# Optimization experiments

Measured on AMD Instinct MI355X. Metric: run time of the kernel, lower is better.

The kernel has to match this reference:

```python
import jax, jax.numpy as jnp
import numpy as np

N_NODES = 50000
N_EDGES = 800000
IN_CH = 128
HID_CH = 128


def glorot(key, shape):
    fan_in, fan_out = shape[0], shape[1]
    lim = np.sqrt(6.0 / (fan_in + fan_out)).astype(np.float32)
    return jax.random.uniform(key, shape, jnp.float32, -lim, lim)


def setup_inputs() -> dict:
    key = jax.random.key(0)
    k1, k2, k3, k4 = jax.random.split(key, 4)
    x = jax.random.normal(k1, (N_NODES, IN_CH), jnp.float32)
    edge_index = jax.random.randint(k2, (2, N_EDGES), 0, N_NODES, jnp.int64)
    W1 = glorot(k3, (IN_CH, HID_CH))
    b1 = jnp.zeros((HID_CH,), jnp.float32)
    W2 = glorot(k4, (HID_CH, HID_CH))
    b2 = jnp.zeros((HID_CH,), jnp.float32)
    return {"x": x, "edge_index": edge_index, "W1": W1, "b1": b1, "W2": W2, "b2": b2}


def _gcn_conv(x, W, b, src, dst, n_nodes):
    # PyG GCNConv: h = D^{-1/2} (A + I) D^{-1/2} (x W) + b
    h = x @ W  # [N, H] transform first (as in PyG)
    loops = jnp.arange(n_nodes, dtype=src.dtype)
    s = jnp.concatenate([src, loops])  # add self-loops
    d = jnp.concatenate([dst, loops])
    deg = jnp.zeros((n_nodes,), h.dtype).at[d].add(1.0)
    dinv = jnp.where(deg > 0, jax.lax.rsqrt(deg), 0.0)
    coef = dinv[s] * dinv[d]  # [E+N]
    msg = h[s] * coef[:, None]  # gather + scale
    out = jax.ops.segment_sum(msg, d, num_segments=n_nodes)  # scatter-add
    return out + b


def reference(x, edge_index, W1, b1, W2, b2):
    src, dst = edge_index[0], edge_index[1]
    n = x.shape[0]
    h = jax.nn.relu(_gcn_conv(x, W1, b1, src, dst, n))
    h = jax.nn.relu(_gcn_conv(h, W2, b2, src, dst, n))
    return h
```

## Files before the change

### kernel.cpp

```cpp
#include <hip/hip_runtime.h>

#define N_NODES 50000
#define N_EDGES 800000
#define CH 128
#define NBUCK 196
#define B_BIN 250
#define CHUNK 3200
#define G_GEMM 782

typedef __attribute__((ext_vector_type(8))) short bf16x8;
typedef __attribute__((ext_vector_type(8))) unsigned short u16x8;
typedef __attribute__((ext_vector_type(4))) float f32x4;

__device__ __forceinline__ float bf2f(unsigned short u) {
    union { unsigned int i; float f; } c;
    c.i = ((unsigned int)u) << 16;
    return c.f;
}
__device__ __forceinline__ unsigned short f2bf(float f) {
    union { float f; unsigned int i; } c;
    c.f = f;
    unsigned int lsb = (c.i >> 16) & 1u;
    c.i += 0x7fffu + lsb;
    return (unsigned short)(c.i >> 16);
}

__global__ __launch_bounds__(256) void k_wt(const float* __restrict__ Wa,
                                            const float* __restrict__ Wb,
                                            unsigned short* __restrict__ Wta,
                                            unsigned short* __restrict__ Wtb) {
    const float* W = blockIdx.x ? Wb : Wa;
    unsigned short* Wt = blockIdx.x ? Wtb : Wta;
    const int tid = threadIdx.x;
    for (int i = 0; i < 64; ++i) {
        int idx = i * 256 + tid;
        int n = idx >> 7, kk = idx & 127;
        Wt[idx] = f2bf(W[kk * CH + n]);
    }
}

__global__ __launch_bounds__(256) void k_mega(
        const int* __restrict__ ei, int* __restrict__ blk_base,
        const float* __restrict__ X, const unsigned short* __restrict__ Wt1,
        unsigned short* __restrict__ HS1u) {
    const int tid = threadIdx.x;
    const int b = blockIdx.x;

    if (b < B_BIN) {
        __shared__ int h[NBUCK];
        for (int i = tid; i < NBUCK; i += 256) h[i] = 0;
        __syncthreads();
        const int e0 = b * CHUNK;
        const int* dst = ei + N_EDGES;
        for (int i = tid; i < CHUNK; i += 256)
            atomicAdd(&h[dst[e0 + i] >> 8], 1);
        __syncthreads();
        for (int k = tid; k < NBUCK; k += 256)
            blk_base[b * NBUCK + k] = h[k];
        return;
    }

    const int gb = b - B_BIN;
    const int l = tid & 63, w = tid >> 6;
    const int lm = l & 15, lk = l >> 4;
    const int row0 = gb * 64 + w * 16;

    int arow = row0 + lm;
    if (arow >= N_NODES) arow = N_NODES - 1;
    bf16x8 a[4];
    #pragma unroll
    for (int ki = 0; ki < 4; ++ki) {
        const float* ap = &X[arow * CH + ki * 32 + lk * 8];
        float4 f0 = *(const float4*)ap;
        float4 f1 = *(const float4*)(ap + 4);
        bf16x8 af;
        af[0] = (short)f2bf(f0.x); af[1] = (short)f2bf(f0.y);
        af[2] = (short)f2bf(f0.z); af[3] = (short)f2bf(f0.w);
        af[4] = (short)f2bf(f1.x); af[5] = (short)f2bf(f1.y);
        af[6] = (short)f2bf(f1.z); af[7] = (short)f2bf(f1.w);
        a[ki] = af;
    }

    #pragma unroll
    for (int ct = 0; ct < 8; ++ct) {
        const unsigned short* wp = &Wt1[(ct * 16 + lm) * CH + lk * 8];
        f32x4 acc = {0.f, 0.f, 0.f, 0.f};
        #pragma unroll
        for (int ki = 0; ki < 4; ++ki) {
            bf16x8 bfrag = *(const bf16x8*)&wp[ki * 32];
            acc = __builtin_amdgcn_mfma_f32_16x16x32_bf16(a[ki], bfrag, acc, 0, 0, 0);
        }
        #pragma unroll
        for (int r = 0; r < 4; ++r) {
            int row = row0 + lk * 4 + r;
            if (row < N_NODES)
                HS1u[row * CH + ct * 16 + lm] = f2bf(acc[r]);
        }
    }
}

__global__ __launch_bounds__(256) void k_colscan(int* __restrict__ blk_base,
                                                 int* __restrict__ bucket_cnt) {
    __shared__ int sm[256];
    const int tid = threadIdx.x, k = blockIdx.x;
    int v = (tid < B_BIN) ? blk_base[tid * NBUCK + k] : 0;
    sm[tid] = v;
    __syncthreads();
    #pragma unroll
    for (int off = 1; off < 256; off <<= 1) {
        int t = (tid >= off) ? sm[tid - off] : 0;
        __syncthreads();
        sm[tid] += t;
        __syncthreads();
    }
    if (tid < B_BIN) blk_base[tid * NBUCK + k] = sm[tid] - v;
    if (tid == 255) bucket_cnt[k] = sm[255];
}

__global__ __launch_bounds__(256) void k_bin_place(const int* __restrict__ ei,
                                                   const int* __restrict__ bucket_cnt,
                                                   const int* __restrict__ blk_base,
                                                   unsigned int* __restrict__ ebuf) {
    __shared__ int sm[256];
    __shared__ int bbase[NBUCK];
    __shared__ int h[NBUCK];
    const int tid = threadIdx.x, b = blockIdx.x;

    int v = (tid < NBUCK) ? bucket_cnt[tid] : 0;
    sm[tid] = v;
    __syncthreads();
    #pragma unroll
    for (int off = 1; off < 256; off <<= 1) {
        int t = (tid >= off) ? sm[tid - off] : 0;
        __syncthreads();
        sm[tid] += t;
        __syncthreads();
    }
    if (tid < NBUCK) bbase[tid] = sm[tid] - v;
    for (int i = tid; i < NBUCK; i += 256) h[i] = 0;
    __syncthreads();

    const int e0 = b * CHUNK;
    for (int i = tid; i < CHUNK; i += 256) {
        int s = ei[e0 + i];
        int d = ei[N_EDGES + e0 + i];
        int k = d >> 8;
        int loc = atomicAdd(&h[k], 1);
        int pos = bbase[k] + blk_base[b * NBUCK + k] + loc;
        ebuf[pos] = ((unsigned int)s << 8) | (unsigned int)(d & 255);
    }
}

__global__ __launch_bounds__(256) void k_bucket_csr(const unsigned int* __restrict__ ebuf,
                                                    const int* __restrict__ bucket_cnt,
                                                    int* __restrict__ rowptr,
                                                    unsigned char* __restrict__ degc,
                                                    int* __restrict__ col) {
    __shared__ int cnts[256];
    __shared__ int fillc[256];
    __shared__ int sm[256];
    __shared__ int e0s;
    const int tid = threadIdx.x, k = blockIdx.x;
    const int node0 = k << 8;

    int vb = (tid < NBUCK) ? bucket_cnt[tid] : 0;
    sm[tid] = vb;
    __syncthreads();
    #pragma unroll
    for (int off = 1; off < 256; off <<= 1) {
        int t = (tid >= off) ? sm[tid - off] : 0;
        __syncthreads();
        sm[tid] += t;
        __syncthreads();
    }
    if (tid == k) e0s = sm[tid] - vb;
    cnts[tid] = 0;
    __syncthreads();
    const int e0 = e0s;
    const int cnt = bucket_cnt[k];

    for (int i = tid; i < cnt; i += 256)
        atomicAdd(&cnts[ebuf[e0 + i] & 255], 1);
    __syncthreads();

    int v = cnts[tid];
    sm[tid] = v;
    __syncthreads();
    #pragma unroll
    for (int off = 1; off < 256; off <<= 1) {
        int t = (tid >= off) ? sm[tid - off] : 0;
        __syncthreads();
        sm[tid] += t;
        __syncthreads();
    }
    int rp = sm[tid] - v;
    fillc[tid] = e0 + rp;
    int node = node0 + tid;
    if (node < N_NODES) {
        rowptr[node] = e0 + rp;
        int dc = v + 1;
        degc[node] = (unsigned char)(dc > 255 ? 255 : dc);
    }
    if (k == NBUCK - 1 && tid == 0) rowptr[N_NODES] = N_EDGES;
    __syncthreads();

    for (int i = tid; i < cnt; i += 256) {
        unsigned int pv = ebuf[e0 + i];
        int loc = atomicAdd(&fillc[pv & 255], 1);
        col[loc] = (int)(pv >> 8);
    }
}

template <int MODE>
__global__ __launch_bounds__(256) void k_agg(
        const int* __restrict__ rowptr, const int* __restrict__ col,
        const unsigned char* __restrict__ degc,
        const unsigned short* __restrict__ H,
        const float* __restrict__ b, unsigned short* __restrict__ OUT) {
    int gid = blockIdx.x * 256 + threadIdx.x;
    int node = gid >> 4;
    if (node >= N_NODES) return;
    int lane = gid & 15;
    const u16x8* H8 = (const u16x8*)H;

    int e0 = rowptr[node];
    int e1 = rowptr[node + 1];
    float di = rsqrtf((float)(e1 - e0 + 1));

    u16x8 hv = H8[node * 16 + lane];
    float acc[8];
    #pragma unroll
    for (int j = 0; j < 8; ++j)
        acc[j] = MODE == 0 ? bf2f(hv[j]) * di : bf2f(hv[j]);

    int e = e0;
    for (; e + 3 < e1; e += 4) {
        int c0 = col[e], c1 = col[e + 1], c2 = col[e + 2], c3 = col[e + 3];
        u16x8 v0 = H8[c0 * 16 + lane];
        u16x8 v1 = H8[c1 * 16 + lane];
        u16x8 v2 = H8[c2 * 16 + lane];
        u16x8 v3 = H8[c3 * 16 + lane];
        if (MODE == 0) {
            float d0 = rsqrtf((float)degc[c0]);
            float d1 = rsqrtf((float)degc[c1]);
            float d2 = rsqrtf((float)degc[c2]);
            float d3 = rsqrtf((float)degc[c3]);
            #pragma unroll
            for (int j = 0; j < 8; ++j)
                acc[j] += (bf2f(v0[j]) * d0 + bf2f(v1[j]) * d1)
                        + (bf2f(v2[j]) * d2 + bf2f(v3[j]) * d3);
        } else {
            #pragma unroll
            for (int j = 0; j < 8; ++j)
                acc[j] += (bf2f(v0[j]) + bf2f(v1[j])) + (bf2f(v2[j]) + bf2f(v3[j]));
        }
    }
    for (; e < e1; ++e) {
        int c0 = col[e];
        u16x8 v = H8[c0 * 16 + lane];
        if (MODE == 0) {
            float ds = rsqrtf((float)degc[c0]);
            #pragma unroll
            for (int j = 0; j < 8; ++j) acc[j] += bf2f(v[j]) * ds;
        } else {
            #pragma unroll
            for (int j = 0; j < 8; ++j) acc[j] += bf2f(v[j]);
        }
    }

    u16x8 o;
    if (MODE == 0) {
        float4 b0 = *(const float4*)&b[lane * 8];
        float4 b1v = *(const float4*)&b[lane * 8 + 4];
        float bb[8] = {b0.x, b0.y, b0.z, b0.w, b1v.x, b1v.y, b1v.z, b1v.w};
        #pragma unroll
        for (int j = 0; j < 8; ++j)
            o[j] = f2bf(fmaxf(acc[j] * di + bb[j], 0.f) * di);
    } else {
        #pragma unroll
        for (int j = 0; j < 8; ++j)
            o[j] = f2bf(acc[j] * di);
    }
    *(u16x8*)&OUT[node * CH + lane * 8] = o;
}

__global__ __launch_bounds__(256) void k_gemm_out(
        const unsigned short* __restrict__ A2,
        const unsigned short* __restrict__ Wt2,
        const float* __restrict__ b2,
        float* __restrict__ OUT) {
    const int tid = threadIdx.x;
    const int l = tid & 63, w = tid >> 6;
    const int lm = l & 15, lk = l >> 4;
    const int row0 = blockIdx.x * 64 + w * 16;

    int arow = row0 + lm;
    if (arow >= N_NODES) arow = N_NODES - 1;
    bf16x8 a[4];
    #pragma unroll
    for (int ki = 0; ki < 4; ++ki)
        a[ki] = *(const bf16x8*)&A2[arow * CH + ki * 32 + lk * 8];

    #pragma unroll
    for (int ct = 0; ct < 8; ++ct) {
        const unsigned short* wp = &Wt2[(ct * 16 + lm) * CH + lk * 8];
        f32x4 acc = {0.f, 0.f, 0.f, 0.f};
        #pragma unroll
        for (int ki = 0; ki < 4; ++ki) {
            bf16x8 bfrag = *(const bf16x8*)&wp[ki * 32];
            acc = __builtin_amdgcn_mfma_f32_16x16x32_bf16(a[ki], bfrag, acc, 0, 0, 0);
        }
        float bb = b2[ct * 16 + lm];
        #pragma unroll
        for (int r = 0; r < 4; ++r) {
            int row = row0 + lk * 4 + r;
            if (row < N_NODES)
                OUT[row * CH + ct * 16 + lm] = fmaxf(acc[r] + bb, 0.f);
        }
    }
}

extern "C" void kernel_launch(void* const* d_in, const int* in_sizes, int n_in,
                              void* d_out, int out_size, void* d_ws, size_t ws_size,
                              hipStream_t stream) {
    const float* x  = (const float*)d_in[0];
    const int*   ei = (const int*)d_in[1];
    const float* W1 = (const float*)d_in[2];
    const float* b1 = (const float*)d_in[3];
    const float* W2 = (const float*)d_in[4];
    const float* b2 = (const float*)d_in[5];
    float* out = (float*)d_out;

    int* blk_base    = (int*)d_ws;
    int* bucket_cnt  = blk_base + 49152;
    int* rowptr      = bucket_cnt + 256;
    unsigned char* degc = (unsigned char*)(rowptr + 50176);
    int* col         = rowptr + 50176 + 12544;
    unsigned int* ebuf = (unsigned int*)(col + 800256);
    unsigned short* hs1u = (unsigned short*)(ebuf + 800256);
    unsigned short* h1p = hs1u + 6400000;
    unsigned short* a2  = h1p + 6400000;
    unsigned short* wt1 = a2 + 6400000;
    unsigned short* wt2 = wt1 + 16384;

    const int gAgg = 3125;

    k_wt<<<2, 256, 0, stream>>>(W1, W2, wt1, wt2);
    k_mega<<<B_BIN + G_GEMM, 256, 0, stream>>>(ei, blk_base, x, wt1, hs1u);
    k_colscan<<<NBUCK, 256, 0, stream>>>(blk_base, bucket_cnt);
    k_bin_place<<<B_BIN, 256, 0, stream>>>(ei, bucket_cnt, blk_base, ebuf);
    k_bucket_csr<<<NBUCK, 256, 0, stream>>>(ebuf, bucket_cnt, rowptr, degc, col);
    k_agg<0><<<gAgg, 256, 0, stream>>>(rowptr, col, degc, hs1u, b1, h1p);
    k_agg<1><<<gAgg, 256, 0, stream>>>(rowptr, col, degc, h1p, nullptr, a2);
    k_gemm_out<<<G_GEMM, 256, 0, stream>>>(a2, wt2, b2, out);
}
```

Before: 142.5 us.

## Sort nodes by degree for load-balanced aggregation and parallelize weight transpose

```diff
diff --git a/kernel.cpp b/kernel.cpp
--- a/kernel.cpp
+++ b/kernel.cpp
@@ -29,14 +29,12 @@
                                             const float* __restrict__ Wb,
                                             unsigned short* __restrict__ Wta,
                                             unsigned short* __restrict__ Wtb) {
-    const float* W = blockIdx.x ? Wb : Wa;
-    unsigned short* Wt = blockIdx.x ? Wtb : Wta;
-    const int tid = threadIdx.x;
-    for (int i = 0; i < 64; ++i) {
-        int idx = i * 256 + tid;
-        int n = idx >> 7, kk = idx & 127;
-        Wt[idx] = f2bf(W[kk * CH + n]);
-    }
+    const int b = blockIdx.x;
+    const float* W = (b & 1) ? Wb : Wa;
+    unsigned short* Wt = (b & 1) ? Wtb : Wta;
+    int idx = (b >> 1) * 256 + threadIdx.x;
+    int n = idx >> 7, kk = idx & 127;
+    Wt[idx] = f2bf(W[kk * CH + n]);
 }
 
 __global__ __launch_bounds__(256) void k_mega(
@@ -100,9 +98,11 @@
 }
 
 __global__ __launch_bounds__(256) void k_colscan(int* __restrict__ blk_base,
-                                                 int* __restrict__ bucket_cnt) {
+                                                 int* __restrict__ bucket_cnt,
+                                                 int* __restrict__ dbin) {
     __shared__ int sm[256];
     const int tid = threadIdx.x, k = blockIdx.x;
+    if (k == 0) dbin[tid] = 0;
     int v = (tid < B_BIN) ? blk_base[tid * NBUCK + k] : 0;
     sm[tid] = v;
     __syncthreads();
@@ -155,7 +155,8 @@
                                                     const int* __restrict__ bucket_cnt,
                                                     int* __restrict__ rowptr,
                                                     unsigned char* __restrict__ degc,
-                                                    int* __restrict__ col) {
+                                                    int* __restrict__ col,
+                                                    int* __restrict__ dbin) {
     __shared__ int cnts[256];
     __shared__ int fillc[256];
     __shared__ int sm[256];
@@ -199,7 +200,9 @@
     if (node < N_NODES) {
         rowptr[node] = e0 + rp;
         int dc = v + 1;
-        degc[node] = (unsigned char)(dc > 255 ? 255 : dc);
+        if (dc > 255) dc = 255;
+        degc[node] = (unsigned char)dc;
+        atomicAdd(&dbin[dc], 1);
     }
     if (k == NBUCK - 1 && tid == 0) rowptr[N_NODES] = N_EDGES;
     __syncthreads();
@@ -211,15 +214,43 @@
     }
 }
 
+__global__ __launch_bounds__(256) void k_degscan(const int* __restrict__ dbin,
+                                                 int* __restrict__ dcur) {
+    __shared__ int sm[256];
+    const int tid = threadIdx.x;
+    int v = dbin[tid];
+    sm[tid] = v;
+    __syncthreads();
+    #pragma unroll
+    for (int off = 1; off < 256; off <<= 1) {
+        int t = (tid >= off) ? sm[tid - off] : 0;
+        __syncthreads();
+        sm[tid] += t;
+        __syncthreads();
+    }
+    dcur[tid] = sm[tid] - v;
+}
+
+__global__ __launch_bounds__(256) void k_degplace(const unsigned char* __restrict__ degc,
+                                                  int* __restrict__ dcur,
+                                                  int* __restrict__ perm) {
+    int node = blockIdx.x * 256 + threadIdx.x;
+    if (node < N_NODES) {
+        int pos = atomicAdd(&dcur[degc[node]], 1);
+        perm[pos] = node;
+    }
+}
+
 template <int MODE>
 __global__ __launch_bounds__(256) void k_agg(
         const int* __restrict__ rowptr, const int* __restrict__ col,
-        const unsigned char* __restrict__ degc,
+        const unsigned char* __restrict__ degc, const int* __restrict__ perm,
         const unsigned short* __restrict__ H,
         const float* __restrict__ b, unsigned short* __restrict__ OUT) {
     int gid = blockIdx.x * 256 + threadIdx.x;
-    int node = gid >> 4;
-    if (node >= N_NODES) return;
+    int g = gid >> 4;
+    if (g >= N_NODES) return;
+    int node = perm[g];
     int lane = gid & 15;
     const u16x8* H8 = (const u16x8*)H;
 
@@ -333,9 +364,12 @@
 
     int* blk_base    = (int*)d_ws;
     int* bucket_cnt  = blk_base + 49152;
-    int* rowptr      = bucket_cnt + 256;
-    unsigned char* degc = (unsigned char*)(rowptr + 50176);
-    int* col         = rowptr + 50176 + 12544;
+    int* dbin        = bucket_cnt + 256;
+    int* dcur        = dbin + 256;
+    int* rowptr      = dcur + 256;
+    int* perm        = rowptr + 50176;
+    unsigned char* degc = (unsigned char*)(perm + 50176);
+    int* col         = perm + 50176 + 12544;
     unsigned int* ebuf = (unsigned int*)(col + 800256);
     unsigned short* hs1u = (unsigned short*)(ebuf + 800256);
     unsigned short* h1p = hs1u + 6400000;
@@ -345,12 +379,14 @@
 
     const int gAgg = 3125;
 
-    k_wt<<<2, 256, 0, stream>>>(W1, W2, wt1, wt2);
+    k_wt<<<128, 256, 0, stream>>>(W1, W2, wt1, wt2);
     k_mega<<<B_BIN + G_GEMM, 256, 0, stream>>>(ei, blk_base, x, wt1, hs1u);
-    k_colscan<<<NBUCK, 256, 0, stream>>>(blk_base, bucket_cnt);
+    k_colscan<<<NBUCK, 256, 0, stream>>>(blk_base, bucket_cnt, dbin);
     k_bin_place<<<B_BIN, 256, 0, stream>>>(ei, bucket_cnt, blk_base, ebuf);
-    k_bucket_csr<<<NBUCK, 256, 0, stream>>>(ebuf, bucket_cnt, rowptr, degc, col);
-    k_agg<0><<<gAgg, 256, 0, stream>>>(rowptr, col, degc, hs1u, b1, h1p);
-    k_agg<1><<<gAgg, 256, 0, stream>>>(rowptr, col, degc, h1p, nullptr, a2);
+    k_bucket_csr<<<NBUCK, 256, 0, stream>>>(ebuf, bucket_cnt, rowptr, degc, col, dbin);
+    k_degscan<<<1, 256, 0, stream>>>(dbin, dcur);
+    k_degplace<<<NBUCK, 256, 0, stream>>>(degc, dcur, perm);
+    k_agg<0><<<gAgg, 256, 0, stream>>>(rowptr, col, degc, perm, hs1u, b1, h1p);
+    k_agg<1><<<gAgg, 256, 0, stream>>>(rowptr, col, degc, perm, h1p, nullptr, a2);
     k_gemm_out<<<G_GEMM, 256, 0, stream>>>(a2, wt2, b2, out);
 }
```

Measured after the change: 417.5 us. 193% more time.
